# Optimization experiments

Hardware: AMD Instinct MI355X
Metric: run time of the kernel (lower is better)

## Reference

```python
import jax, jax.numpy as jnp
import numpy as np

NUM_SELECT = 300
OUT_H = 448
OUT_W = 448


def setup_inputs() -> dict:
    key = jax.random.key(0)
    k1, k2, k3 = jax.random.split(key, 3)
    B, Q, C = 4, 900, 91
    pred_logits = jax.random.normal(k1, (B, Q, C), dtype=jnp.float32)
    pred_boxes = jax.random.uniform(k2, (B, Q, 4), dtype=jnp.float32)  # cxcywh in [0,1)
    pred_masks = jax.random.normal(k3, (B, Q, 28, 28), dtype=jnp.float32)
    # all images same size so resize output shape is static under jit
    target_sizes = jnp.full((B, 2), OUT_H, dtype=jnp.int64 if jax.config.jax_enable_x64 else jnp.int32)
    return {"pred_logits": pred_logits, "pred_boxes": pred_boxes,
            "pred_masks": pred_masks, "target_sizes": target_sizes}


def _box_cxcywh_to_xyxy(b):
    cx, cy, w, h = jnp.split(b, 4, axis=-1)
    return jnp.concatenate([cx - 0.5 * w, cy - 0.5 * h, cx + 0.5 * w, cy + 0.5 * h], axis=-1)


def reference(pred_logits, pred_boxes, pred_masks, target_sizes):
    B, Q, C = pred_logits.shape
    # sigmoid + topk over flattened (query, class) axis
    prob = jax.nn.sigmoid(pred_logits).reshape(B, Q * C)
    scores, topk_idx = jax.lax.top_k(prob, NUM_SELECT)          # [B, K]
    topk_boxes = topk_idx // C                                   # query index [B, K]
    labels = topk_idx % C                                        # class index [B, K]

    boxes = _box_cxcywh_to_xyxy(pred_boxes)                      # [B, Q, 4]
    boxes = jnp.take_along_axis(boxes, topk_boxes[:, :, None], axis=1)  # [B, K, 4]

    img_h = target_sizes[:, 0].astype(boxes.dtype)
    img_w = target_sizes[:, 1].astype(boxes.dtype)
    scale = jnp.stack([img_w, img_h, img_w, img_h], axis=1)      # [B, 4]
    boxes = boxes * scale[:, None, :]

    # gather top-k masks: [B, K, 28, 28]
    masks = jnp.take_along_axis(pred_masks, topk_boxes[:, :, None, None], axis=1)
    masks = masks.astype(jnp.float16)
    # bilinear, half-pixel centers == torch align_corners=False
    resize_one = lambda m: jax.image.resize(m, (NUM_SELECT, OUT_H, OUT_W), method="bilinear")
    masks = jax.vmap(resize_one)(masks)                          # [B, K, OUT_H, OUT_W] fp16

    return scores, labels, boxes, masks
```

## Files before the change

### kernel.cpp

```cpp
#include <hip/hip_runtime.h>
#include <hip/hip_fp16.h>

#define QN 900
#define CN 91
#define TOTN (QN * CN)
#define KSEL 300
#define BN 4
#define OUTW 448
#define MASKPIX (OUTW * OUTW)
#define OFFS_LABELS (BN * KSEL)
#define OFFS_BOXES  (2 * BN * KSEL)
#define OFFS_MASKS  (6 * BN * KSEL)
#define MAXC 2048
#define BT 1024

typedef float floatx4 __attribute__((ext_vector_type(4)));

static __device__ __forceinline__ unsigned fkey(float f) {
    unsigned u = __float_as_uint(f);
    return (u & 0x80000000u) ? ~u : (u | 0x80000000u);
}

__global__ __launch_bounds__(BT) void select_kernel(
    const float* __restrict__ logits, const float* __restrict__ boxes,
    const int* __restrict__ tsz, float* out, int* qsel)
{
    const int b = blockIdx.x;
    const int tid = threadIdx.x;
    const int lane = tid & 63;
    const float* lg = logits + (size_t)b * TOTN;

    __shared__ unsigned hlane[256 * 33];
    __shared__ unsigned hist[256];
    __shared__ int sh_bin, sh_want, sh_chunk;
    __shared__ unsigned sh_above, sh_cnt;
    __shared__ int cidx[MAXC];
    __shared__ unsigned ckey[MAXC];

    for (int i = tid; i < 256 * 33; i += BT) hlane[i] = 0;
    __syncthreads();
    {
        const int sl = lane & 31;
        for (int i = tid; i < TOTN; i += BT) {
            unsigned key = fkey(lg[i]);
            atomicAdd(&hlane[(key >> 24) * 33 + sl], 1u);
        }
    }
    __syncthreads();
    if (tid < 256) {
        unsigned s = 0;
#pragma unroll
        for (int l = 0; l < 32; ++l) s += hlane[tid * 33 + l];
        hist[tid] = s;
    }
    __syncthreads();

    unsigned prefix = 0;
    int want = KSEL;
#pragma unroll
    for (int round = 0; round < 2; ++round) {
        const int shift = 24 - 8 * round;
        if (round > 0) {
            if (tid < 256) hist[tid] = 0;
            __syncthreads();
            for (int i = tid; i < TOTN; i += BT) {
                unsigned key = fkey(lg[i]);
                if ((key & 0xFF000000u) == prefix)
                    atomicAdd(&hist[(key >> 16) & 255u], 1u);
            }
            __syncthreads();
        }
        if (tid < 64) {
            unsigned p = hist[tid * 4] + hist[tid * 4 + 1]
                       + hist[tid * 4 + 2] + hist[tid * 4 + 3];
            unsigned suffix = p;
#pragma unroll
            for (int o = 1; o < 64; o <<= 1) {
                unsigned t = __shfl_down(suffix, o);
                if (tid + o < 64) suffix += t;
            }
            unsigned nxt = __shfl_down(suffix, 1);
            if (tid == 63) nxt = 0;
            bool flag = (suffix >= (unsigned)want) && (nxt < (unsigned)want);
            if (flag) { sh_chunk = tid; sh_above = nxt; }
        }
        __syncthreads();
        if (tid == 0) {
            int ch = sh_chunk;
            unsigned acc = sh_above;
            int j = 3;
            for (; j > 0; --j) {
                if (acc + hist[ch * 4 + j] >= (unsigned)want) break;
                acc += hist[ch * 4 + j];
            }
            sh_bin = ch * 4 + j;
            sh_want = want - (int)acc;
        }
        __syncthreads();
        prefix |= ((unsigned)sh_bin << shift);
        want = sh_want;
        __syncthreads();
    }
    const unsigned T16 = prefix >> 16;

    if (tid == 0) sh_cnt = 0;
    __syncthreads();
    for (int i = tid; i < TOTN; i += BT) {
        unsigned key = fkey(lg[i]);
        if ((key >> 16) >= T16) {
            unsigned p = atomicAdd(&sh_cnt, 1u);
            if (p < MAXC) { cidx[p] = i; ckey[p] = key; }
        }
    }
    __syncthreads();
    const int ncand = min((int)sh_cnt, MAXC);

    const float fh = (float)tsz[b * 2 + 0];
    const float fw = (float)tsz[b * 2 + 1];

    for (int c = tid; c < ncand; c += BT) {
        const unsigned kc = ckey[c];
        const int ic = cidx[c];
        int rank = 0;
        for (int s = 0; s < ncand; ++s) {
            unsigned ks = ckey[s];
            if (ks > kc || (ks == kc && cidx[s] < ic)) ++rank;
        }
        if (rank < KSEL) {
            float lf = lg[ic];
            float score = 1.0f / (1.0f + expf(-lf));
            int q = ic / CN;
            int label = ic - q * CN;

            out[b * KSEL + rank] = score;
            out[OFFS_LABELS + b * KSEL + rank] = (float)label;

            const float* bx = boxes + ((size_t)b * QN + q) * 4;
            float cx = bx[0], cy = bx[1], ww = bx[2], hh = bx[3];
            float* ob = out + OFFS_BOXES + ((size_t)(b * KSEL + rank)) * 4;
            ob[0] = (cx - 0.5f * ww) * fw;
            ob[1] = (cy - 0.5f * hh) * fh;
            ob[2] = (cx + 0.5f * ww) * fw;
            ob[3] = (cy + 0.5f * hh) * fh;

            qsel[b * KSEL + rank] = q;
        }
    }
}

#define SPLIT 4
#define ROWSB (OUTW / SPLIT)

__global__ __launch_bounds__(256) void mask_kernel(
    const float* __restrict__ masks, const int* __restrict__ qsel,
    float* __restrict__ out)
{
    const int mk = blockIdx.x >> 2;
    const int part = blockIdx.x & 3;
    const int b = mk / KSEL;
    const int q = qsel[mk];
    const float* __restrict__ src = masks + ((size_t)b * QN + q) * 784;

    const int j = threadIdx.x & 127;
    const int rhalf = threadIdx.x >> 7;
    if (j >= 112) return;

    const int qd = j & 3;
    const int i4 = j >> 2;
    const int c0 = i4 - 1 + (qd >> 1);
    const int c0c = c0 < 0 ? 0 : c0;
    const int c1c = (c0 + 1 > 27) ? 27 : c0 + 1;
    const float toff = 0.25f * (float)qd - ((qd >= 2) ? 1.0f : 0.0f);
    const float t0 = 0.53125f + toff, t1 = 0.59375f + toff,
                t2 = 0.65625f + toff, t3 = 0.71875f + toff;

    const int ystart = part * ROWSB + rhalf;
    float* optr = out + OFFS_MASKS + (size_t)mk * MASKPIX
                + (size_t)ystart * OUTW + j * 4;

    float sy = (float)ystart * 0.0625f - 0.46875f;
    int prev_iy = -1000;
    float m00 = 0.f, m01 = 0.f, d0 = 0.f, d1 = 0.f;

#pragma unroll 2
    for (int k = 0; k < ROWSB / 2; ++k) {
        float yf = floorf(sy);
        float ty = sy - yf;
        int iy = (int)yf;
        if (iy != prev_iy) {
            prev_iy = iy;
            int y0 = iy < 0 ? 0 : iy;
            int y1 = (iy + 1 > 27) ? 27 : iy + 1;
            float a0 = src[y0 * 28 + c0c];
            float a1 = src[y0 * 28 + c1c];
            float b0 = src[y1 * 28 + c0c];
            float b1 = src[y1 * 28 + c1c];
            m00 = a0; m01 = a1;
            d0 = b0 - a0; d1 = b1 - a1;
        }
        float v0 = fmaf(ty, d0, m00);
        float v1 = fmaf(ty, d1, m01);
        float dv = v1 - v0;
        floatx4 w;
        w.x = fmaf(t0, dv, v0);
        w.y = fmaf(t1, dv, v0);
        w.z = fmaf(t2, dv, v0);
        w.w = fmaf(t3, dv, v0);
        *reinterpret_cast<floatx4*>(optr) = w;
        optr += 2 * OUTW;
        sy += 0.125f;
    }
}

extern "C" void kernel_launch(void* const* d_in, const int* in_sizes, int n_in,
                              void* d_out, int out_size, void* d_ws, size_t ws_size,
                              hipStream_t stream) {
    const float* pred_logits = (const float*)d_in[0];
    const float* pred_boxes  = (const float*)d_in[1];
    const float* pred_masks  = (const float*)d_in[2];
    const int*   target_sz   = (const int*)d_in[3];
    float* out = (float*)d_out;
    int* qsel = (int*)d_ws;

    select_kernel<<<BN, BT, 0, stream>>>(pred_logits, pred_boxes, target_sz, out, qsel);
    mask_kernel<<<BN * KSEL * SPLIT, 256, 0, stream>>>(pred_masks, qsel, out);
}
```

Baseline: 270.5 us.

## Split first-pass top-k histogram across multiple blocks per batch

Moves the first radix-histogram pass over the logits out of the single-block-per-batch selection kernel into a separate kernel with four blocks per batch. Each block writes its partial histogram to workspace, and the selection kernel sums them before continuing. This is meant to spread the first full scan of 81900 elements over more CUs. The cost is an extra kernel launch and a global-memory round trip for the partial histograms.

```diff
diff --git a/kernel.cpp b/kernel.cpp
--- a/kernel.cpp
+++ b/kernel.cpp
@@ -14,6 +14,9 @@
 #define MAXC 2048
 #define BT 1024
 
+#define APB 4
+#define AELEM (TOTN / APB)
+
 typedef float floatx4 __attribute__((ext_vector_type(4)));
 
 static __device__ __forceinline__ unsigned fkey(float f) {
@@ -21,36 +24,47 @@
     return (u & 0x80000000u) ? ~u : (u | 0x80000000u);
 }
 
-__global__ __launch_bounds__(BT) void select_kernel(
+__global__ __launch_bounds__(1024) void hist_part(
+    const float* __restrict__ logits, unsigned* __restrict__ wsh)
+{
+    const int b = blockIdx.x >> 2, part = blockIdx.x & 3;
+    const int tid = threadIdx.x;
+    const float* lg = logits + (size_t)b * TOTN + (size_t)part * AELEM;
+
+    __shared__ unsigned h[256 * 9];
+    for (int i = tid; i < 256 * 9; i += 1024) h[i] = 0;
+    __syncthreads();
+    const int sl = tid & 7;
+    for (int i = tid; i < AELEM; i += 1024)
+        atomicAdd(&h[(fkey(lg[i]) >> 24) * 9 + sl], 1u);
+    __syncthreads();
+    if (tid < 256) {
+        unsigned s = 0;
+#pragma unroll
+        for (int k = 0; k < 8; ++k) s += h[tid * 9 + k];
+        wsh[blockIdx.x * 256 + tid] = s;
+    }
+}
+
+__global__ __launch_bounds__(BT) void select_final(
     const float* __restrict__ logits, const float* __restrict__ boxes,
-    const int* __restrict__ tsz, float* out, int* qsel)
+    const int* __restrict__ tsz, const unsigned* __restrict__ wsh,
+    float* out, int* qsel)
 {
     const int b = blockIdx.x;
     const int tid = threadIdx.x;
-    const int lane = tid & 63;
     const float* lg = logits + (size_t)b * TOTN;
 
-    __shared__ unsigned hlane[256 * 33];
     __shared__ unsigned hist[256];
     __shared__ int sh_bin, sh_want, sh_chunk;
     __shared__ unsigned sh_above, sh_cnt;
     __shared__ int cidx[MAXC];
     __shared__ unsigned ckey[MAXC];
 
-    for (int i = tid; i < 256 * 33; i += BT) hlane[i] = 0;
-    __syncthreads();
-    {
-        const int sl = lane & 31;
-        for (int i = tid; i < TOTN; i += BT) {
-            unsigned key = fkey(lg[i]);
-            atomicAdd(&hlane[(key >> 24) * 33 + sl], 1u);
-        }
-    }
-    __syncthreads();
     if (tid < 256) {
         unsigned s = 0;
 #pragma unroll
-        for (int l = 0; l < 32; ++l) s += hlane[tid * 33 + l];
+        for (int p = 0; p < APB; ++p) s += wsh[(b * APB + p) * 256 + tid];
         hist[tid] = s;
     }
     __syncthreads();
@@ -221,7 +235,10 @@
     const int*   target_sz   = (const int*)d_in[3];
     float* out = (float*)d_out;
     int* qsel = (int*)d_ws;
-
-    select_kernel<<<BN, BT, 0, stream>>>(pred_logits, pred_boxes, target_sz, out, qsel);
+    unsigned* wsh = (unsigned*)((char*)d_ws + 5120);
+
+    hist_part<<<BN * APB, 1024, 0, stream>>>(pred_logits, wsh);
+    select_final<<<BN, BT, 0, stream>>>(pred_logits, pred_boxes, target_sz,
+                                        wsh, out, qsel);
     mask_kernel<<<BN * KSEL * SPLIT, 256, 0, stream>>>(pred_masks, qsel, out);
 }
```

Measured after the change: 254.7 us. 1.06x faster.
